# Kernel tuning notes

Hardware: AMD Instinct MI355X
Metric: run time of the kernel (lower is better)

## Reference

```python
import jax, jax.numpy as jnp
import numpy as np
import math

HIDDEN = 1024
HEADS = 16
HEAD_DIM = HIDDEN // HEADS


def setup_inputs() -> dict:
    key = jax.random.key(0)
    k1, k2, k3, k4, k5 = jax.random.split(key, 5)
    B, S = 2, 2048
    scale = 1.0 / math.sqrt(HIDDEN)
    return {
        "batch_hidden": jax.random.normal(k1, (B, S, HIDDEN), dtype=jnp.float32),
        # nn.Linear weights are [out, in]; y = x @ W.T
        "Wq": jax.random.uniform(k2, (HIDDEN, HIDDEN), jnp.float32, -scale, scale),
        "Wk": jax.random.uniform(k3, (HIDDEN, HIDDEN), jnp.float32, -scale, scale),
        "Wg": jax.random.uniform(k4, (HIDDEN, HIDDEN), jnp.float32, -scale, scale),
        "bg": jax.random.uniform(k5, (HIDDEN,), jnp.float32, -scale, scale),
    }


def _split_heads(x):
    # [B,S,H] -> [B,heads,S,head_dim]
    B, S, _ = x.shape
    return x.reshape(B, S, HEADS, HEAD_DIM).transpose(0, 2, 1, 3)


def reference(batch_hidden, Wq, Wk, Wg, bg):
    # NOTE: faithful to source — value uses the KEY projection weights.
    q = batch_hidden @ Wq.T
    k = batch_hidden @ Wk.T
    v = batch_hidden @ Wk.T
    gate = jax.nn.sigmoid(batch_hidden @ Wg.T + bg)  # [B,S,H]

    q = _split_heads(q)  # [B,h,S,d]
    k = _split_heads(k)
    v = _split_heads(v)

    # source: scores = K @ Q^T (softmax over query positions)
    scores = jnp.einsum("bhkd,bhqd->bhkq", k, q) / math.sqrt(HEAD_DIM)
    attn = jax.nn.softmax(scores, axis=-1)  # [B,h,S,S]

    ctx = jnp.einsum("bhkq,bhqd->bhkd", attn, v)  # [B,h,S,d]
    ctx = ctx.transpose(0, 2, 1, 3).reshape(batch_hidden.shape)  # [B,S,H]

    out = gate * ctx
    return out, attn
```

## Files before the change

### kernel.cpp

```cpp
#include <hip/hip_runtime.h>
#include <hip/hip_bf16.h>

#define HID 1024
#define NHEADS 16
#define HDIM 64
#define SEQ 2048
#define NTOK 4096

typedef __attribute__((ext_vector_type(8))) short short8;
typedef __attribute__((ext_vector_type(4))) float f32x4;
typedef unsigned short ush;

__device__ __forceinline__ ush f2bf(float f) {
    unsigned int u = __float_as_uint(f);
    u = (u + 0x7fffu + ((u >> 16) & 1u)) >> 16;
    return (ush)u;
}
__device__ __forceinline__ void async_copy16(const void* g, void* l) {
    __builtin_amdgcn_global_load_lds(
        (const __attribute__((address_space(1))) void*)g,
        (__attribute__((address_space(3))) void*)l, 16, 0, 0);
}
#define SBAR()  __builtin_amdgcn_s_barrier()
#define SCHED() __builtin_amdgcn_sched_barrier(0)

__global__ __launch_bounds__(256) void cvt_kernel(
    const float* __restrict__ X, const float* __restrict__ Wq,
    const float* __restrict__ Wk, const float* __restrict__ Wg,
    ush* __restrict__ Xbf, ush* __restrict__ Wbf)
{
    long i = (long)blockIdx.x * 256 + threadIdx.x;
    const float* src; ush* dst; long j;
    if (i < 524288)      { src = X;  dst = Xbf;           j = i; }
    else if (i < 655360) { src = Wq; dst = Wbf;           j = i - 524288; }
    else if (i < 786432) { src = Wk; dst = Wbf + 1048576; j = i - 655360; }
    else                 { src = Wg; dst = Wbf + 2097152; j = i - 786432; }
    float4 a = *reinterpret_cast<const float4*>(src + j * 8);
    float4 b = *reinterpret_cast<const float4*>(src + j * 8 + 4);
    short8 o;
    o[0] = (short)f2bf(a.x); o[1] = (short)f2bf(a.y);
    o[2] = (short)f2bf(a.z); o[3] = (short)f2bf(a.w);
    o[4] = (short)f2bf(b.x); o[5] = (short)f2bf(b.y);
    o[6] = (short)f2bf(b.z); o[7] = (short)f2bf(b.w);
    *reinterpret_cast<short8*>(dst + j * 8) = o;
}

__global__ __launch_bounds__(256, 3) void proj_kernel(
    const ush* __restrict__ Xbf, const ush* __restrict__ Wbf,
    const float* __restrict__ bgp,
    ush* __restrict__ Qbf, ush* __restrict__ Kbf,
    ush* __restrict__ VtG,
    float* __restrict__ gate)
{
    __shared__ __align__(16) ush As[128 * 64];
    __shared__ __align__(16) ush Bs[128 * 64];

    const int lin = blockIdx.y * 24 + blockIdx.x;
    const int swz = (lin & 7) * 96 + (lin >> 3);
    const int n0 = (swz % 24) * 128;
    const int m0 = (swz / 24) * 128;
    const int tid = threadIdx.x, lane = tid & 63, wv = tid >> 6;
    const int wm = wv >> 1, wn = wv & 1;
    const int l16 = lane & 15, lq = lane >> 4;
    const int lrow = lane >> 3, lc = lane & 7;
    const int scU = lc ^ lrow;
    const int u0 = lq ^ (l16 & 7);

    f32x4 acc[4][4];
    #pragma unroll
    for (int i = 0; i < 4; i++)
        #pragma unroll
        for (int j = 0; j < 4; j++)
            #pragma unroll
            for (int r = 0; r < 4; r++) acc[i][j][r] = 0.0f;

    const ush* gA = Xbf + (long)m0 * HID;
    const ush* gB = Wbf + (long)n0 * HID;

    for (int k0 = 0; k0 < HID; k0 += 64) {
        #pragma unroll
        for (int c = 0; c < 4; ++c) {
            int chunk = wv * 4 + c;
            int row = chunk * 8 + lrow;
            async_copy16(gA + (long)row * HID + k0 + scU * 8, &As[chunk * 512]);
            async_copy16(gB + (long)row * HID + k0 + scU * 8, &Bs[chunk * 512]);
        }
        asm volatile("s_waitcnt vmcnt(0)" ::: "memory");
        SCHED();
        SBAR(); SCHED();
        #pragma unroll
        for (int ks = 0; ks < 2; ++ks) {
            const int uo = (ks ? (u0 ^ 4) : u0) * 8;
            short8 a[4], b[4];
            #pragma unroll
            for (int mf = 0; mf < 4; mf++)
                a[mf] = *reinterpret_cast<const short8*>(&As[(wm * 64 + mf * 16 + l16) * 64 + uo]);
            #pragma unroll
            for (int nf = 0; nf < 4; nf++)
                b[nf] = *reinterpret_cast<const short8*>(&Bs[(wn * 64 + nf * 16 + l16) * 64 + uo]);
            #pragma unroll
            for (int mf = 0; mf < 4; mf++)
                #pragma unroll
                for (int nf = 0; nf < 4; nf++)
                    acc[mf][nf] = __builtin_amdgcn_mfma_f32_16x16x32_bf16(a[mf], b[nf], acc[mf][nf], 0, 0, 0);
        }
        SBAR(); SCHED();
    }

    const int z = n0 >> 10;
    #pragma unroll
    for (int mf = 0; mf < 4; mf++)
        #pragma unroll
        for (int nf = 0; nf < 4; nf++) {
            int row = m0 + wm * 64 + mf * 16 + lq * 4;
            int gcol = n0 + wn * 64 + nf * 16 + l16;
            int col = gcol & 1023;
            #pragma unroll
            for (int r = 0; r < 4; r++) {
                float v = acc[mf][nf][r];
                long idx = (long)(row + r) * HID + col;
                if (z == 0)      Qbf[idx] = f2bf(v * 0.18033688011112042f);
                else if (z == 1) Kbf[idx] = f2bf(v);
                else {
                    float gv = 1.0f / (1.0f + __expf(-(v + bgp[col])));
                    __builtin_nontemporal_store(gv, &gate[idx]);
                }
            }
            if (z == 1) {
                int bb = row >> 11, s = row & 2047;
                int bh = bb * NHEADS + (col >> 6);
                int d  = col & 63;
                unsigned int w0, w1;
                asm volatile("v_cvt_pk_bf16_f32 %0, %1, %2" : "=v"(w0)
                             : "v"(acc[mf][nf][0]), "v"(acc[mf][nf][1]));
                asm volatile("v_cvt_pk_bf16_f32 %0, %1, %2" : "=v"(w1)
                             : "v"(acc[mf][nf][2]), "v"(acc[mf][nf][3]));
                *reinterpret_cast<uint2*>(&VtG[((long)bh * HDIM + d) * SEQ + s]) =
                    make_uint2(w0, w1);
            }
        }
}

__global__ __launch_bounds__(256, 2) void attn_kernel(
    const ush* __restrict__ Qbf,
    const ush* __restrict__ Kbf,
    const ush* __restrict__ VtG,
    float* __restrict__ outp,
    float* __restrict__ attnp)
{
    __shared__ __align__(16) ush QsA[3 * 4096];
    __shared__ __align__(16) ush AtA[64 * 72];
    __shared__ __align__(16) ush VtA[64 * 64];

    ush (*At)[72] = reinterpret_cast<ush(*)[72]>(&AtA[0]);

    const int lin  = blockIdx.x;
    const int swzb = (lin & 7) * 64 + (lin >> 3);
    const int rh   = swzb & 1;
    const int pair = (swzb >> 1) & 7;
    const int h    = (swzb >> 4) & 15;
    const int b    = swzb >> 8;
    const int bh   = b * NHEADS + h;
    const int tb   = b * SEQ;
    const int colbase = h * HDIM;
    const int rowbase_a = pair * 256 + rh * 64;
    const int rowbase_b = rowbase_a + 128;

    const int tid  = threadIdx.x;
    const int lane = tid & 63;
    const int wv   = tid >> 6;
    const int l16  = lane & 15, lq = lane >> 4;
    const int u0   = lq ^ (l16 & 7);
    const int rlo  = lane >> 4;
    const int qc2  = (lane & 15) * 4;

    auto stageT = [&](const ush* src, long stride, ush* dst) {
        #pragma unroll
        for (int c = 0; c < 2; ++c) {
            int p = c * 256 + tid;
            int row = p >> 3, lc2 = p & 7;
            int scU2 = lc2 ^ (row & 7);
            async_copy16(src + (long)row * stride + scU2 * 8, dst + c * 2048 + wv * 512);
        }
    };
    const ush* Qsrc = Qbf + (long)tb * HID + colbase;
    const ush* Vsrc = VtG + (long)bh * HDIM * SEQ;

    short8 bk_a[2], bk_b[2];
    {
        stageT(Kbf + (long)(tb + rowbase_a) * HID + colbase, HID, AtA);
        asm volatile("s_waitcnt vmcnt(0)" ::: "memory"); SCHED();
        SBAR(); SCHED();
        #pragma unroll
        for (int ks = 0; ks < 2; ++ks) {
            const int uo = (ks ? (u0 ^ 4) : u0) * 8;
            bk_a[ks] = *reinterpret_cast<const short8*>(&AtA[(wv * 16 + l16) * 64 + uo]);
        }
        SBAR(); SCHED();
        stageT(Kbf + (long)(tb + rowbase_b) * HID + colbase, HID, AtA);
        asm volatile("s_waitcnt vmcnt(0)" ::: "memory"); SCHED();
        SBAR(); SCHED();
        #pragma unroll
        for (int ks = 0; ks < 2; ++ks) {
            const int uo = (ks ? (u0 ^ 4) : u0) * 8;
            bk_b[ks] = *reinterpret_cast<const short8*>(&AtA[(wv * 16 + l16) * 64 + uo]);
        }
        SBAR(); SCHED();
    }

    stageT(Qsrc, HID, &QsA[0]);
    stageT(Qsrc + (long)64 * HID, HID, &QsA[4096]);

    float ps_a = 0.0f;
    for (int i = 0; i < 32; ++i) {
        if (i >= 30) asm volatile("s_waitcnt vmcnt(0)" ::: "memory");
        else         asm volatile("s_waitcnt vmcnt(2)" ::: "memory");
        SCHED();
        SBAR(); SCHED();
        if (i < 30) stageT(Qsrc + (long)((i + 2) * 64) * HID, HID, &QsA[((i + 2) % 3) * 4096]);

        f32x4 acc[4];
        #pragma unroll
        for (int x = 0; x < 4; x++)
            #pragma unroll
            for (int r = 0; r < 4; r++) acc[x][r] = 0.0f;

        const ush* Qb = &QsA[(i % 3) * 4096];
        __builtin_amdgcn_s_setprio(1);
        #pragma unroll
        for (int ks = 0; ks < 2; ks++) {
            const int uo = (ks ? (u0 ^ 4) : u0) * 8;
            short8 aq[4];
            #pragma unroll
            for (int mf = 0; mf < 4; mf++)
                aq[mf] = *reinterpret_cast<const short8*>(&Qb[(mf * 16 + l16) * 64 + uo]);
            #pragma unroll
            for (int mf = 0; mf < 4; mf++)
                acc[mf] = __builtin_amdgcn_mfma_f32_16x16x32_bf16(aq[mf], bk_a[ks], acc[mf], 0, 0, 0);
        }
        __builtin_amdgcn_s_setprio(0);

        #pragma unroll
        for (int mf = 0; mf < 4; mf++) {
            float s = 0.0f;
            #pragma unroll
            for (int r = 0; r < 4; r++) s += exp2f(acc[mf][r]);
            ps_a += s;
        }
    }
    float inv_a;
    {
        float v = ps_a;
        v += __shfl_xor(v, 16);
        v += __shfl_xor(v, 32);
        inv_a = 1.0f / v;
    }

    SBAR();
    stageT(Qsrc, HID, &QsA[0]);
    stageT(Vsrc, SEQ, VtA);
    stageT(Qsrc + (long)64 * HID, HID, &QsA[4096]);

    float ps_b = 0.0f;
    f32x4 octx[4];
    #pragma unroll
    for (int y = 0; y < 4; y++)
        #pragma unroll
        for (int r = 0; r < 4; r++) octx[y][r] = 0.0f;

    for (int i = 0; i < 32; ++i) {
        const int q0 = i << 6;
        if (i == 0) asm volatile("s_waitcnt vmcnt(0)" ::: "memory");
        else        asm volatile("s_waitcnt vmcnt(4)" ::: "memory");
        SCHED();
        SBAR(); SCHED();
        if (i < 30) stageT(Qsrc + (long)((i + 2) * 64) * HID, HID, &QsA[((i + 2) % 3) * 4096]);

        f32x4 aA[4], aB[4];
        #pragma unroll
        for (int x = 0; x < 4; x++)
            #pragma unroll
            for (int r = 0; r < 4; r++) { aA[x][r] = 0.0f; aB[x][r] = 0.0f; }

        const ush* Qb = &QsA[(i % 3) * 4096];
        __builtin_amdgcn_s_setprio(1);
        #pragma unroll
        for (int ks = 0; ks < 2; ks++) {
            const int uo = (ks ? (u0 ^ 4) : u0) * 8;
            short8 aq[4];
            #pragma unroll
            for (int mf = 0; mf < 4; mf++)
                aq[mf] = *reinterpret_cast<const short8*>(&Qb[(mf * 16 + l16) * 64 + uo]);
            #pragma unroll
            for (int mf = 0; mf < 4; mf++)
                aA[mf] = __builtin_amdgcn_mfma_f32_16x16x32_bf16(aq[mf], bk_a[ks], aA[mf], 0, 0, 0);
            #pragma unroll
            for (int mf = 0; mf < 4; mf++)
                aB[mf] = __builtin_amdgcn_mfma_f32_16x16x32_bf16(aq[mf], bk_b[ks], aB[mf], 0, 0, 0);
        }
        __builtin_amdgcn_s_setprio(0);

        {
            const int krl = wv * 16 + l16;
            #pragma unroll
            for (int mf = 0; mf < 4; mf++) {
                const int qc = mf * 16 + lq * 4;
                float p0 = exp2f(aA[mf][0]) * inv_a;
                float p1 = exp2f(aA[mf][1]) * inv_a;
                float p2 = exp2f(aA[mf][2]) * inv_a;
                float p3 = exp2f(aA[mf][3]) * inv_a;
                unsigned int w0, w1;
                asm volatile("v_cvt_pk_bf16_f32 %0, %1, %2" : "=v"(w0) : "v"(p0), "v"(p1));
                asm volatile("v_cvt_pk_bf16_f32 %0, %1, %2" : "=v"(w1) : "v"(p2), "v"(p3));
                *reinterpret_cast<uint2*>(&At[krl][qc]) = make_uint2(w0, w1);
            }
        }
        asm volatile("s_waitcnt lgkmcnt(0)" ::: "memory");
        SCHED();

        uint2 wreg[4];
        #pragma unroll
        for (int j = 0; j < 4; ++j)
            wreg[j] = *reinterpret_cast<const uint2*>(&At[wv * 16 + j * 4 + rlo][qc2]);

        __builtin_amdgcn_s_setprio(1);
        #pragma unroll
        for (int ks = 0; ks < 2; ks++) {
            const int uo = (ks ? (u0 ^ 4) : u0) * 8;
            short8 a = *reinterpret_cast<const short8*>(&At[wv * 16 + l16][ks * 32 + lq * 8]);
            #pragma unroll
            for (int nf = 0; nf < 4; nf++) {
                short8 bv = *reinterpret_cast<const short8*>(&VtA[(nf * 16 + l16) * 64 + uo]);
                octx[nf] = __builtin_amdgcn_mfma_f32_16x16x32_bf16(a, bv, octx[nf], 0, 0, 0);
            }
        }
        __builtin_amdgcn_s_setprio(0);

        #pragma unroll
        for (int mf = 0; mf < 4; mf++) {
            float s = 0.0f;
            #pragma unroll
            for (int r = 0; r < 4; r++) s += exp2f(aB[mf][r]);
            ps_b += s;
        }

        SBAR(); SCHED();
        if (i < 31) stageT(Vsrc + (i + 1) * 64, SEQ, VtA);

        #pragma unroll
        for (int j = 0; j < 4; ++j) {
            const int rl = rowbase_a + wv * 16 + j * 4 + rlo;
            f32x4 st;
            st[0] = __uint_as_float(wreg[j].x << 16);
            st[1] = __uint_as_float(wreg[j].x & 0xffff0000u);
            st[2] = __uint_as_float(wreg[j].y << 16);
            st[3] = __uint_as_float(wreg[j].y & 0xffff0000u);
            __builtin_nontemporal_store(st,
                reinterpret_cast<f32x4*>(attnp + ((long)bh * SEQ + rl) * SEQ + q0 + qc2));
        }
    }
    float inv_b;
    {
        float v = ps_b;
        v += __shfl_xor(v, 16);
        v += __shfl_xor(v, 32);
        inv_b = 1.0f / v;
    }

    #pragma unroll
    for (int nf = 0; nf < 4; nf++) {
        int col = colbase + nf * 16 + l16;
        #pragma unroll
        for (int r = 0; r < 4; r++) {
            long idx = (long)(tb + rowbase_a + wv * 16 + lq * 4 + r) * HID + col;
            float g = __builtin_nontemporal_load(&outp[idx]);
            __builtin_nontemporal_store(g * octx[nf][r], &outp[idx]);
        }
    }

    stageT(Qsrc, HID, &QsA[0]);
    stageT(Vsrc, SEQ, VtA);
    stageT(Qsrc + (long)64 * HID, HID, &QsA[4096]);

    #pragma unroll
    for (int y = 0; y < 4; y++)
        #pragma unroll
        for (int r = 0; r < 4; r++) octx[y][r] = 0.0f;

    for (int i = 0; i < 32; ++i) {
        const int q0 = i << 6;
        if (i == 0) asm volatile("s_waitcnt vmcnt(0)" ::: "memory");
        else        asm volatile("s_waitcnt vmcnt(4)" ::: "memory");
        SCHED();
        SBAR(); SCHED();
        if (i < 30) stageT(Qsrc + (long)((i + 2) * 64) * HID, HID, &QsA[((i + 2) % 3) * 4096]);

        f32x4 aB[4];
        #pragma unroll
        for (int x = 0; x < 4; x++)
            #pragma unroll
            for (int r = 0; r < 4; r++) aB[x][r] = 0.0f;

        const ush* Qb = &QsA[(i % 3) * 4096];
        __builtin_amdgcn_s_setprio(1);
        #pragma unroll
        for (int ks = 0; ks < 2; ks++) {
            const int uo = (ks ? (u0 ^ 4) : u0) * 8;
            short8 aq[4];
            #pragma unroll
            for (int mf = 0; mf < 4; mf++)
                aq[mf] = *reinterpret_cast<const short8*>(&Qb[(mf * 16 + l16) * 64 + uo]);
            #pragma unroll
            for (int mf = 0; mf < 4; mf++)
                aB[mf] = __builtin_amdgcn_mfma_f32_16x16x32_bf16(aq[mf], bk_b[ks], aB[mf], 0, 0, 0);
        }
        __builtin_amdgcn_s_setprio(0);

        {
            const int krl = wv * 16 + l16;
            #pragma unroll
            for (int mf = 0; mf < 4; mf++) {
                const int qc = mf * 16 + lq * 4;
                float p0 = exp2f(aB[mf][0]) * inv_b;
                float p1 = exp2f(aB[mf][1]) * inv_b;
                float p2 = exp2f(aB[mf][2]) * inv_b;
                float p3 = exp2f(aB[mf][3]) * inv_b;
                unsigned int w0, w1;
                asm volatile("v_cvt_pk_bf16_f32 %0, %1, %2" : "=v"(w0) : "v"(p0), "v"(p1));
                asm volatile("v_cvt_pk_bf16_f32 %0, %1, %2" : "=v"(w1) : "v"(p2), "v"(p3));
                *reinterpret_cast<uint2*>(&At[krl][qc]) = make_uint2(w0, w1);
            }
        }
        asm volatile("s_waitcnt lgkmcnt(0)" ::: "memory");
        SCHED();

        uint2 wreg[4];
        #pragma unroll
        for (int j = 0; j < 4; ++j)
            wreg[j] = *reinterpret_cast<const uint2*>(&At[wv * 16 + j * 4 + rlo][qc2]);

        __builtin_amdgcn_s_setprio(1);
        #pragma unroll
        for (int ks = 0; ks < 2; ks++) {
            const int uo = (ks ? (u0 ^ 4) : u0) * 8;
            short8 a = *reinterpret_cast<const short8*>(&At[wv * 16 + l16][ks * 32 + lq * 8]);
            #pragma unroll
            for (int nf = 0; nf < 4; nf++) {
                short8 bv = *reinterpret_cast<const short8*>(&VtA[(nf * 16 + l16) * 64 + uo]);
                octx[nf] = __builtin_amdgcn_mfma_f32_16x16x32_bf16(a, bv, octx[nf], 0, 0, 0);
            }
        }
        __builtin_amdgcn_s_setprio(0);

        SBAR(); SCHED();
        if (i < 31) stageT(Vsrc + (i + 1) * 64, SEQ, VtA);

        #pragma unroll
        for (int j = 0; j < 4; ++j) {
            const int rl = rowbase_b + wv * 16 + j * 4 + rlo;
            f32x4 st;
            st[0] = __uint_as_float(wreg[j].x << 16);
            st[1] = __uint_as_float(wreg[j].x & 0xffff0000u);
            st[2] = __uint_as_float(wreg[j].y << 16);
            st[3] = __uint_as_float(wreg[j].y & 0xffff0000u);
            __builtin_nontemporal_store(st,
                reinterpret_cast<f32x4*>(attnp + ((long)bh * SEQ + rl) * SEQ + q0 + qc2));
        }
    }

    #pragma unroll
    for (int nf = 0; nf < 4; nf++) {
        int col = colbase + nf * 16 + l16;
        #pragma unroll
        for (int r = 0; r < 4; r++) {
            long idx = (long)(tb + rowbase_b + wv * 16 + lq * 4 + r) * HID + col;
            float g = __builtin_nontemporal_load(&outp[idx]);
            __builtin_nontemporal_store(g * octx[nf][r], &outp[idx]);
        }
    }
}

extern "C" void kernel_launch(void* const* d_in, const int* in_sizes, int n_in,
                              void* d_out, int out_size, void* d_ws, size_t ws_size,
                              hipStream_t stream)
{
    const float* X  = (const float*)d_in[0];
    const float* Wq = (const float*)d_in[1];
    const float* Wk = (const float*)d_in[2];
    const float* Wg = (const float*)d_in[3];
    const float* bg = (const float*)d_in[4];

    float* outp  = (float*)d_out;
    float* attnp = outp + (long)NTOK * HID;

    ush* Qbf = (ush*)d_ws;
    ush* Kbf = Qbf + (long)NTOK * HID;
    ush* VtG = Kbf + (long)NTOK * HID;

    ush* Xbf = (ush*)(outp + 134742016L);
    ush* Wbf = Xbf + (long)NTOK * HID;

    cvt_kernel<<<3584, 256, 0, stream>>>(X, Wq, Wk, Wg, Xbf, Wbf);
    proj_kernel<<<dim3(24, 32), 256, 0, stream>>>(Xbf, Wbf, bg, Qbf, Kbf, VtG, outp);
    attn_kernel<<<512, 256, 0, stream>>>(Qbf, Kbf, VtG, outp, attnp);
}
```

Before: 206.2 us.

## Triple-buffer V tiles alongside Q to drop the mid-iteration barrier

V tiles move from a single shared-memory buffer to a 3-deep ring, matching the Q buffers, and are prefetched two iterations ahead together with Q. The second barrier and the V reload partway through each loop iteration are removed, and the vmcnt waits are adjusted for the larger number of loads in flight. The aim is fewer block-wide syncs and V load latency hidden behind compute. The cost is 16 KB more LDS per block, which may press on the two-blocks-per-CU occupancy target.

```diff
diff --git a/kernel.cpp b/kernel.cpp
--- a/kernel.cpp
+++ b/kernel.cpp
@@ -150,7 +150,7 @@
 {
     __shared__ __align__(16) ush QsA[3 * 4096];
     __shared__ __align__(16) ush AtA[64 * 72];
-    __shared__ __align__(16) ush VtA[64 * 64];
+    __shared__ __align__(16) ush VtA[3 * 4096];
 
     ush (*At)[72] = reinterpret_cast<ush(*)[72]>(&AtA[0]);
 
@@ -258,8 +258,9 @@
 
     SBAR();
     stageT(Qsrc, HID, &QsA[0]);
-    stageT(Vsrc, SEQ, VtA);
+    stageT(Vsrc, SEQ, &VtA[0]);
     stageT(Qsrc + (long)64 * HID, HID, &QsA[4096]);
+    stageT(Vsrc + 64, SEQ, &VtA[4096]);
 
     float ps_b = 0.0f;
     f32x4 octx[4];
@@ -270,11 +271,16 @@
 
     for (int i = 0; i < 32; ++i) {
         const int q0 = i << 6;
-        if (i == 0) asm volatile("s_waitcnt vmcnt(0)" ::: "memory");
-        else        asm volatile("s_waitcnt vmcnt(4)" ::: "memory");
+        if (i == 0)       asm volatile("s_waitcnt vmcnt(4)"  ::: "memory");
+        else if (i == 1)  asm volatile("s_waitcnt vmcnt(8)"  ::: "memory");
+        else if (i == 31) asm volatile("s_waitcnt vmcnt(8)"  ::: "memory");
+        else              asm volatile("s_waitcnt vmcnt(12)" ::: "memory");
         SCHED();
         SBAR(); SCHED();
-        if (i < 30) stageT(Qsrc + (long)((i + 2) * 64) * HID, HID, &QsA[((i + 2) % 3) * 4096]);
+        if (i < 30) {
+            stageT(Qsrc + (long)((i + 2) * 64) * HID, HID, &QsA[((i + 2) % 3) * 4096]);
+            stageT(Vsrc + (i + 2) * 64, SEQ, &VtA[((i + 2) % 3) * 4096]);
+        }
 
         f32x4 aA[4], aB[4];
         #pragma unroll
@@ -323,6 +329,7 @@
         for (int j = 0; j < 4; ++j)
             wreg[j] = *reinterpret_cast<const uint2*>(&At[wv * 16 + j * 4 + rlo][qc2]);
 
+        const ush* Vb = &VtA[(i % 3) * 4096];
         __builtin_amdgcn_s_setprio(1);
         #pragma unroll
         for (int ks = 0; ks < 2; ks++) {
@@ -330,7 +337,7 @@
             short8 a = *reinterpret_cast<const short8*>(&At[wv * 16 + l16][ks * 32 + lq * 8]);
             #pragma unroll
             for (int nf = 0; nf < 4; nf++) {
-                short8 bv = *reinterpret_cast<const short8*>(&VtA[(nf * 16 + l16) * 64 + uo]);
+                short8 bv = *reinterpret_cast<const short8*>(&Vb[(nf * 16 + l16) * 64 + uo]);
                 octx[nf] = __builtin_amdgcn_mfma_f32_16x16x32_bf16(a, bv, octx[nf], 0, 0, 0);
             }
         }
@@ -343,9 +350,6 @@
             for (int r = 0; r < 4; r++) s += exp2f(aB[mf][r]);
             ps_b += s;
         }
-
-        SBAR(); SCHED();
-        if (i < 31) stageT(Vsrc + (i + 1) * 64, SEQ, VtA);
 
         #pragma unroll
         for (int j = 0; j < 4; ++j) {
@@ -378,9 +382,11 @@
         }
     }
 
+    SBAR();
     stageT(Qsrc, HID, &QsA[0]);
-    stageT(Vsrc, SEQ, VtA);
+    stageT(Vsrc, SEQ, &VtA[0]);
     stageT(Qsrc + (long)64 * HID, HID, &QsA[4096]);
+    stageT(Vsrc + 64, SEQ, &VtA[4096]);
 
     #pragma unroll
     for (int y = 0; y < 4; y++)
@@ -389,11 +395,16 @@
 
     for (int i = 0; i < 32; ++i) {
         const int q0 = i << 6;
-        if (i == 0) asm volatile("s_waitcnt vmcnt(0)" ::: "memory");
-        else        asm volatile("s_waitcnt vmcnt(4)" ::: "memory");
+        if (i == 0)       asm volatile("s_waitcnt vmcnt(4)"  ::: "memory");
+        else if (i == 1)  asm volatile("s_waitcnt vmcnt(8)"  ::: "memory");
+        else if (i == 31) asm volatile("s_waitcnt vmcnt(8)"  ::: "memory");
+        else              asm volatile("s_waitcnt vmcnt(12)" ::: "memory");
         SCHED();
         SBAR(); SCHED();
-        if (i < 30) stageT(Qsrc + (long)((i + 2) * 64) * HID, HID, &QsA[((i + 2) % 3) * 4096]);
+        if (i < 30) {
+            stageT(Qsrc + (long)((i + 2) * 64) * HID, HID, &QsA[((i + 2) % 3) * 4096]);
+            stageT(Vsrc + (i + 2) * 64, SEQ, &VtA[((i + 2) % 3) * 4096]);
+        }
 
         f32x4 aB[4];
         #pragma unroll
@@ -439,6 +450,7 @@
         for (int j = 0; j < 4; ++j)
             wreg[j] = *reinterpret_cast<const uint2*>(&At[wv * 16 + j * 4 + rlo][qc2]);
 
+        const ush* Vb = &VtA[(i % 3) * 4096];
         __builtin_amdgcn_s_setprio(1);
         #pragma unroll
         for (int ks = 0; ks < 2; ks++) {
@@ -446,14 +458,11 @@
             short8 a = *reinterpret_cast<const short8*>(&At[wv * 16 + l16][ks * 32 + lq * 8]);
             #pragma unroll
             for (int nf = 0; nf < 4; nf++) {
-                short8 bv = *reinterpret_cast<const short8*>(&VtA[(nf * 16 + l16) * 64 + uo]);
+                short8 bv = *reinterpret_cast<const short8*>(&Vb[(nf * 16 + l16) * 64 + uo]);
                 octx[nf] = __builtin_amdgcn_mfma_f32_16x16x32_bf16(a, bv, octx[nf], 0, 0, 0);
             }
         }
         __builtin_amdgcn_s_setprio(0);
-
-        SBAR(); SCHED();
-        if (i < 31) stageT(Vsrc + (i + 1) * 64, SEQ, VtA);
 
         #pragma unroll
         for (int j = 0; j < 4; ++j) {
```

Result: no change. 206.9 us (median of 2 runs) (+0.4%).
